# Performance work log

Measured on AMD Instinct MI355X. Metric: run time of the kernel, lower is better.

## Reference

```python
import jax, jax.numpy as jnp
import numpy as np

G = 200          # voxel grid extent per axis (spatial_shape)
EPS = 1e-5       # BatchNorm eps


def setup_inputs() -> dict:
    N, C_in, C_out = 1_000_000, 6, 32
    rng = np.random.default_rng(0)
    # unique active voxel sites (submanifold conv assumes deduplicated coords)
    lin = rng.choice(G ** 3, size=N, replace=False)
    coords = np.stack([lin // (G * G), (lin // G) % G, lin % G], axis=1).astype(np.int32)
    key = jax.random.key(0)
    k1, k2 = jax.random.split(key)
    feat = jax.random.normal(k1, (N, C_in), jnp.float32)
    W = jax.random.normal(k2, (27, C_in, C_out), jnp.float32) * (1.0 / np.sqrt(27 * C_in))
    gamma = jnp.ones((C_out,), jnp.float32)
    beta = jnp.zeros((C_out,), jnp.float32)
    return {"feat": feat, "coords": jnp.asarray(coords), "W": W, "gamma": gamma, "beta": beta}


def _subm_conv_bn_relu(feat, coords, W, gamma, beta):
    # Submanifold 3x3x3 sparse conv: output only at active sites.
    N = feat.shape[0]
    c = coords
    keys = (c[:, 0] * G + c[:, 1]) * G + c[:, 2]          # linearized voxel keys
    order = jnp.argsort(keys)
    skeys = keys[order]
    sfeat = feat[order]
    # all 27 kernel offsets, center included
    r = jnp.arange(-1, 2, dtype=c.dtype)
    offs = jnp.stack(jnp.meshgrid(r, r, r, indexing="ij"), -1).reshape(27, 3)

    def step(acc, xs):
        off, Wk = xs                                       # off: [3], Wk: [C_in, C_out]
        nc = c + off                                       # neighbor coords [N,3]
        valid = jnp.all((nc >= 0) & (nc < G), axis=1)
        nkey = (nc[:, 0] * G + nc[:, 1]) * G + nc[:, 2]
        pos = jnp.clip(jnp.searchsorted(skeys, nkey), 0, N - 1)
        found = valid & (skeys[pos] == nkey)               # rulebook hit mask
        g = jnp.where(found[:, None], sfeat[pos], 0.0)     # gathered neighbor feats [N,C_in]
        return acc + g @ Wk, None

    out, _ = jax.lax.scan(step, jnp.zeros((N, W.shape[2]), feat.dtype), (offs, W))
    # BatchNorm1d (training-mode batch stats) + ReLU
    mean = out.mean(0)
    var = out.var(0)
    out = (out - mean) * jax.lax.rsqrt(var + EPS) * gamma + beta
    return jax.nn.relu(out)


def reference(feat, coords, W, gamma, beta):
    return _subm_conv_bn_relu(feat, coords, W, gamma, beta)
```

## Files before the change

kernel.cpp:

```cpp
#include <hip/hip_runtime.h>
#include <stdint.h>

#define GRIDX 200
#define P 202
#define PCELL (P * P * P)
#define GUARD 100000
#define NBITS (PCELL + GUARD)
#define NWP ((NBITS + 31) / 32)
#define K_INV (PCELL + 50000)
#define CIN 6
#define COUT 32
#define NOFF 27
#define BN_EPS 1e-5f
#define WPB 1024
#define NBLKP ((NWP + WPB - 1) / WPB)

typedef __attribute__((ext_vector_type(8))) short short8;
typedef __attribute__((ext_vector_type(4))) float f32x4;


__device__ __forceinline__ int xcd_swizzle(int b, int nwg) {
    int q = nwg >> 3, r = nwg & 7;
    int xcd = b & 7, idx = b >> 3;
    int base = (xcd < r) ? xcd * (q + 1) : r * (q + 1) + (xcd - r) * q;
    return base + idx;
}

__device__ __forceinline__ unsigned short f2bf(float f) {
    uint32_t u = __float_as_uint(f);
    return (unsigned short)((u + 0x7FFFu + ((u >> 16) & 1u)) >> 16);
}
__device__ __forceinline__ uint32_t pack2(float a, float b) {
    return (uint32_t)f2bf(a) | ((uint32_t)f2bf(b) << 16);
}
__device__ __forceinline__ float bflo(uint32_t u) { return __uint_as_float(u << 16); }
__device__ __forceinline__ float bfhi(uint32_t u) { return __uint_as_float(u & 0xFFFF0000u); }

__device__ __forceinline__ int koff_delta(int koff) {
    int t9 = koff / 9;
    int r9 = koff - t9 * 9;
    int t3 = r9 / 3;
    return (t9 - 1) * (P * P) + (t3 - 1) * P + (r9 - t3 * 3 - 1);
}


__global__ __launch_bounds__(256)
void build_bitmap_v4(const int* __restrict__ coords, int N, uint2* __restrict__ recs) {
    int t = blockIdx.x * blockDim.x + threadIdx.x;
    int i0 = t * 4;
    if (i0 >= N) return;
    if (i0 + 4 <= N) {
        const int4* c4 = (const int4*)(coords + (size_t)i0 * 3);
        int4 ca = c4[0], cb = c4[1], cc = c4[2];
        int cx[4] = {ca.x, ca.w, cb.z, cc.y};
        int cy[4] = {ca.y, cb.x, cb.w, cc.z};
        int cz[4] = {ca.z, cb.y, cc.x, cc.w};
#pragma unroll
        for (int s = 0; s < 4; s++) {
            int key = ((cx[s] + 1) * P + (cy[s] + 1)) * P + (cz[s] + 1);
            atomicOr((unsigned int*)&recs[key >> 5], 1u << (key & 31));
        }
    } else {
        for (int i = i0; i < N; i++) {
            int x = coords[3 * i], y = coords[3 * i + 1], z = coords[3 * i + 2];
            int key = ((x + 1) * P + (y + 1)) * P + (z + 1);
            atomicOr((unsigned int*)&recs[key >> 5], 1u << (key & 31));
        }
    }
}

__global__ __launch_bounds__(256)
void bitmap_count_p(const uint2* __restrict__ recs, int* __restrict__ bcnt) {
    __shared__ int tot[256];
    int b = blockIdx.x, t = threadIdx.x;
    int w0 = b * WPB + t * 4;
    int s = 0;
#pragma unroll
    for (int j = 0; j < 4; j++) {
        int w = w0 + j;
        if (w < NWP) s += __popc(recs[w].x);
    }
    tot[t] = s;
    __syncthreads();
    if (t < 128) tot[t] += tot[t + 128];
    __syncthreads();
    if (t < 64) {
        int v = tot[t] + tot[t + 64];
#pragma unroll
        for (int d = 32; d > 0; d >>= 1) v += __shfl_down(v, d);
        if (t == 0) bcnt[b] = v;
    }
}

__global__ void scan_small(const int* __restrict__ cnt, int* __restrict__ base, int n) {
    __shared__ int tot[256];
    int t = threadIdx.x;
    int v = (t < n) ? cnt[t] : 0;
    tot[t] = v;
    __syncthreads();
    for (int d = 1; d < 256; d <<= 1) {
        int u = (t >= d) ? tot[t - d] : 0;
        __syncthreads();
        tot[t] += u;
        __syncthreads();
    }
    if (t < n) base[t] = tot[t] - v;
}

__global__ __launch_bounds__(256)
void base_fill_skeys(uint2* __restrict__ recs, const int* __restrict__ bbase,
                     int* __restrict__ skeys) {
    __shared__ int tot[256];
    int b = blockIdx.x, t = threadIdx.x;
    int w0 = b * WPB + t * 4;
    uint32_t wd[4];
    int p[4];
    int s = 0;
#pragma unroll
    for (int j = 0; j < 4; j++) {
        int w = w0 + j;
        wd[j] = (w < NWP) ? recs[w].x : 0u;
        p[j] = __popc(wd[j]);
        s += p[j];
    }
    tot[t] = s;
    __syncthreads();
    for (int d = 1; d < 256; d <<= 1) {
        int u = (t >= d) ? tot[t - d] : 0;
        __syncthreads();
        tot[t] += u;
        __syncthreads();
    }
    int run = bbase[b] + tot[t] - s;
#pragma unroll
    for (int j = 0; j < 4; j++) {
        int w = w0 + j;
        if (w < NWP) {
            recs[w].y = (uint32_t)run;
            uint32_t m = wd[j];
            int rr = run;
            int k0 = w * 32;
            while (m) {
                int bit = __ffs((int)m) - 1;
                skeys[rr++] = k0 + bit;
                m &= m - 1u;
            }
            run += p[j];
        }
    }
}


__global__ __launch_bounds__(256)
void rank_scatter_v4(const int* __restrict__ coords, const float* __restrict__ feat, int N,
                     const uint2* __restrict__ recs,
                     uint4* __restrict__ rec32) {
    int t = blockIdx.x * blockDim.x + threadIdx.x;
    int i0 = t * 4;
    if (i0 >= N) return;
    if (i0 + 4 <= N) {
        const int4* c4 = (const int4*)(coords + (size_t)i0 * 3);
        int4 ca = c4[0], cb = c4[1], cc = c4[2];
        int cx[4] = {ca.x, ca.w, cb.z, cc.y};
        int cy[4] = {ca.y, cb.x, cb.w, cc.z};
        int cz[4] = {ca.z, cb.y, cc.x, cc.w};
        const float4* f4 = (const float4*)(feat + (size_t)i0 * 6);
        float4 fa = f4[0], fb = f4[1], fc = f4[2], fd = f4[3], fe = f4[4], ff = f4[5];
        float fs[4][6] = {
            {fa.x, fa.y, fa.z, fa.w, fb.x, fb.y},
            {fb.z, fb.w, fc.x, fc.y, fc.z, fc.w},
            {fd.x, fd.y, fd.z, fd.w, fe.x, fe.y},
            {fe.z, fe.w, ff.x, ff.y, ff.z, ff.w}};
#pragma unroll
        for (int s = 0; s < 4; s++) {
            int key = ((cx[s] + 1) * P + (cy[s] + 1)) * P + (cz[s] + 1);
            uint2 rb = recs[key >> 5];
            int bit = key & 31;
            int r = (int)(rb.y + (uint32_t)__popc(rb.x & ((1u << bit) - 1u)));
            uint4 u;
            u.x = pack2(fs[s][0], fs[s][1]);
            u.y = pack2(fs[s][2], fs[s][3]);
            u.z = pack2(fs[s][4], fs[s][5]);
            u.w = 0u;
            rec32[(size_t)r * 2] = u;
            ((uint32_t*)&rec32[(size_t)r * 2 + 1])[0] = (uint32_t)(i0 + s);
        }
    } else {
        for (int i = i0; i < N; i++) {
            int x = coords[3 * i], y = coords[3 * i + 1], z = coords[3 * i + 2];
            int key = ((x + 1) * P + (y + 1)) * P + (z + 1);
            uint2 rb = recs[key >> 5];
            int bit = key & 31;
            int r = (int)(rb.y + (uint32_t)__popc(rb.x & ((1u << bit) - 1u)));
            const float* fr = feat + (size_t)i * CIN;
            uint4 u;
            u.x = pack2(fr[0], fr[1]);
            u.y = pack2(fr[2], fr[3]);
            u.z = pack2(fr[4], fr[5]);
            u.w = 0u;
            rec32[(size_t)r * 2] = u;
            ((uint32_t*)&rec32[(size_t)r * 2 + 1])[0] = (uint32_t)i;
        }
    }
}


__global__ void prep_wfrag(const float* __restrict__ W, uint4* __restrict__ wfrag) {
    int idx = blockIdx.x * blockDim.x + threadIdx.x;
    if (idx >= 7 * 2 * 64) return;
    int l = idx & 63;
    int nt = (idx >> 6) & 1;
    int ks = idx >> 7;
    int koff = (l >> 4) * 7 + ks;
    int col = nt * 16 + (l & 15);
    unsigned short v[8];
#pragma unroll
    for (int ci = 0; ci < 8; ci++) {
        float f = 0.f;
        if (ci < CIN && koff < NOFF) f = W[(koff * CIN + ci) * COUT + col];
        v[ci] = f2bf(f);
    }
    uint4 u;
    u.x = (uint32_t)v[0] | ((uint32_t)v[1] << 16);
    u.y = (uint32_t)v[2] | ((uint32_t)v[3] << 16);
    u.z = (uint32_t)v[4] | ((uint32_t)v[5] << 16);
    u.w = (uint32_t)v[6] | ((uint32_t)v[7] << 16);
    wfrag[idx] = u;
}


__global__ __launch_bounds__(256, 4)
void conv_mfma(const uint4* __restrict__ rec32,
               const int* __restrict__ skeys,
               const uint4* __restrict__ wfrag,
               const uint2* __restrict__ recs, int N, int nsb,
               uint4* __restrict__ wsbf,
               float* __restrict__ stats_g) {
    __shared__ __align__(16) float Clds[64 * 36];
    __shared__ float bstat[64];

    int tid = threadIdx.x;
    int w = tid >> 6, l = tid & 63;
    int col = l & 15;
    int rg = l >> 4;
    int kb = rg;

    if (tid < 64) bstat[tid] = 0.f;

    const short8* wf8 = (const short8*)wfrag;
    short8 bf0[7], bf1[7];
#pragma unroll
    for (int ks = 0; ks < 7; ks++) {
        bf0[ks] = wf8[(ks * 2 + 0) * 64 + l];
        bf1[ks] = wf8[(ks * 2 + 1) * 64 + l];
    }

    int b1 = (0x3123 >> (kb * 4)) & 0xF;
    int b2 = b1 + 3;
    int len0 = b1, len2 = 4 - b1;
    int koffC0 = kb * 7;
    int koffC1 = koffC0 + b1;
    int koffC2 = koffC0 + b2;
    int d0 = koff_delta(koffC0);
    int d1 = koff_delta(koffC1);
    bool padC2 = (koffC2 >= NOFF);
    int d2 = padC2 ? 0 : koff_delta(koffC2);

    float as0 = 0.f, aq0 = 0.f, as1 = 0.f, aq1 = 0.f;

    for (int sb = blockIdx.x; sb < nsb; sb += gridDim.x) {
        int b = xcd_swizzle(sb, nsb);
        int bs = b * 64;
        int site = bs + w * 16 + col;
        int key = (site < N) ? skeys[site] : K_INV;

        int nkA = key + d0;
        int nkB = key + d1;
        int nkC = padC2 ? K_INV : key + d2;
        int waA = nkA >> 5, waB = nkB >> 5, waC = nkC >> 5;
        uint2 rA0 = recs[waA];
        uint2 rB0 = recs[waB];
        uint2 rC0 = recs[waC];
        uint2 rA1 = rA0, rB1 = rB0, rC1 = rC0;
        if (((nkA & 31) + len0) > 32) rA1 = recs[waA + 1];
        if (((nkB & 31) + 3) > 32)    rB1 = recs[waB + 1];
        if (((nkC & 31) + len2) > 32) rC1 = recs[waC + 1];

        short8 av[7];
#pragma unroll
        for (int ks = 0; ks < 7; ks++) {
            int c = (ks >= b1) + (ks >= b2);
            int nk = (c == 0) ? (nkA + ks)
                   : (c == 1) ? (nkB + (ks - b1))
                              : (nkC + (ks - b2));
            int wa  = (c == 0) ? waA : (c == 1) ? waB : waC;
            uint2 r0 = (c == 0) ? rA0 : (c == 1) ? rB0 : rC0;
            uint2 r1 = (c == 0) ? rA1 : (c == 1) ? rB1 : rC1;
            bool second = (nk >> 5) != wa;
            uint32_t wd = second ? r1.x : r0.x;
            uint32_t bw = second ? r1.y : r0.y;
            int p = nk & 31;
            bool hit = (wd >> p) & 1u;
            uint4 a4 = make_uint4(0u, 0u, 0u, 0u);
            if (hit) {
                int pos = (int)(bw + (uint32_t)__popc(wd & ((1u << p) - 1u)));
                a4 = rec32[(size_t)pos * 2];
            }
            av[ks] = *(const short8*)&a4;
        }

        f32x4 acc0 = {0.f, 0.f, 0.f, 0.f};
        f32x4 acc1 = {0.f, 0.f, 0.f, 0.f};
#pragma unroll
        for (int ks = 0; ks < 7; ks++) {
            acc0 = __builtin_amdgcn_mfma_f32_16x16x32_bf16(av[ks], bf0[ks], acc0, 0, 0, 0);
            acc1 = __builtin_amdgcn_mfma_f32_16x16x32_bf16(av[ks], bf1[ks], acc1, 0, 0, 0);
        }

        as0 += acc0[0] + acc0[1] + acc0[2] + acc0[3];
        aq0 += acc0[0]*acc0[0] + acc0[1]*acc0[1] + acc0[2]*acc0[2] + acc0[3]*acc0[3];
        as1 += acc1[0] + acc1[1] + acc1[2] + acc1[3];
        aq1 += acc1[0]*acc1[0] + acc1[1]*acc1[1] + acc1[2]*acc1[2] + acc1[3]*acc1[3];

        __syncthreads();
#pragma unroll
        for (int r = 0; r < 4; r++) {
            int s = w * 16 + rg * 4 + r;
            Clds[s * 36 + col] = acc0[r];
            Clds[s * 36 + col + 16] = acc1[r];
        }
        __syncthreads();

        int st = tid >> 2;
        int q = tid & 3;
        int sr = bs + st;
        if (sr < N) {
            uint32_t orig = ((const uint32_t*)rec32)[(size_t)sr * 8 + 4];
            const float* cp = &Clds[st * 36 + q * 8];
            uint4 v;
            v.x = pack2(cp[0], cp[1]);
            v.y = pack2(cp[2], cp[3]);
            v.z = pack2(cp[4], cp[5]);
            v.w = pack2(cp[6], cp[7]);
            wsbf[(size_t)orig * 4 + q] = v;
        }
    }

    as0 += __shfl_xor(as0, 16); as0 += __shfl_xor(as0, 32);
    aq0 += __shfl_xor(aq0, 16); aq0 += __shfl_xor(aq0, 32);
    as1 += __shfl_xor(as1, 16); as1 += __shfl_xor(as1, 32);
    aq1 += __shfl_xor(aq1, 16); aq1 += __shfl_xor(aq1, 32);
    __syncthreads();
    if (l < 16) {
        atomicAdd(&bstat[col], as0);
        atomicAdd(&bstat[16 + col], as1);
        atomicAdd(&bstat[32 + col], aq0);
        atomicAdd(&bstat[48 + col], aq1);
    }
    __syncthreads();
    if (tid < 64) {
        int slice = blockIdx.x & 63;
        atomicAdd(&stats_g[slice * 64 + tid], bstat[tid]);
    }
}


__global__ void finalize_sliced(const float* __restrict__ stats_g,
                                const float* __restrict__ gamma,
                                const float* __restrict__ beta,
                                float invN, float* __restrict__ scsh) {
    int c = threadIdx.x;
    if (c < COUT) {
        float s = 0.f, q = 0.f;
        for (int sl = 0; sl < 64; sl++) {
            s += stats_g[sl * 64 + c];
            q += stats_g[sl * 64 + 32 + c];
        }
        float mean = s * invN;
        float var = q * invN - mean * mean;
        float sc = gamma[c] * rsqrtf(var + BN_EPS);
        scsh[c] = sc;
        scsh[COUT + c] = beta[c] - mean * sc;
    }
}


__global__ __launch_bounds__(256)
void norm_bf(const uint4* __restrict__ wsbf, int N,
             const float* __restrict__ scsh, float* __restrict__ out) {
    __shared__ float sc[COUT], sh[COUT];
    for (int t = threadIdx.x; t < COUT; t += blockDim.x) {
        sc[t] = scsh[t];
        sh[t] = scsh[COUT + t];
    }
    __syncthreads();
    int tid = blockIdx.x * blockDim.x + threadIdx.x;
    int i = tid >> 2, q = tid & 3;
    if (i >= N) return;
    uint4 v = wsbf[(size_t)i * 4 + q];
    int cb = q * 8;
    float4 o0, o1;
    o0.x = fmaxf(bflo(v.x) * sc[cb + 0] + sh[cb + 0], 0.f);
    o0.y = fmaxf(bfhi(v.x) * sc[cb + 1] + sh[cb + 1], 0.f);
    o0.z = fmaxf(bflo(v.y) * sc[cb + 2] + sh[cb + 2], 0.f);
    o0.w = fmaxf(bfhi(v.y) * sc[cb + 3] + sh[cb + 3], 0.f);
    o1.x = fmaxf(bflo(v.z) * sc[cb + 4] + sh[cb + 4], 0.f);
    o1.y = fmaxf(bfhi(v.z) * sc[cb + 5] + sh[cb + 5], 0.f);
    o1.z = fmaxf(bflo(v.w) * sc[cb + 6] + sh[cb + 6], 0.f);
    o1.w = fmaxf(bfhi(v.w) * sc[cb + 7] + sh[cb + 7], 0.f);
    float4* gp = (float4*)(out + (size_t)i * COUT + cb);
    gp[0] = o0;
    gp[1] = o1;
}


extern "C" void kernel_launch(void* const* d_in, const int* in_sizes, int n_in,
                              void* d_out, int out_size, void* d_ws, size_t ws_size,
                              hipStream_t stream) {
    const float* feat   = (const float*)d_in[0];
    const int*   coords = (const int*)d_in[1];
    const float* W      = (const float*)d_in[2];
    const float* gamma  = (const float*)d_in[3];
    const float* beta   = (const float*)d_in[4];
    float* out = (float*)d_out;

    int N = in_sizes[0] / CIN;
    const int threads = 256;
    int blocks4 = (N + 4 * threads - 1) / (4 * threads);
    int nsb = (N + 63) / 64;
    int cblocks = 1024;
    int nblocks = (4 * N + threads - 1) / threads;

    size_t a256 = 255;
    size_t recs_b     = (size_t)NWP * 8;
    size_t off_stats  = (recs_b + a256) & ~a256;
    size_t zero_bytes = off_stats + (size_t)64 * 64 * 4;
    size_t off_scsh   = (zero_bytes + a256) & ~a256;
    size_t off_skeys  = (off_scsh + 2 * COUT * 4 + a256) & ~a256;
    size_t off_rec32  = (off_skeys + (size_t)N * 4 + a256) & ~a256;
    size_t off_bcnt   = (off_rec32 + (size_t)(N + 1) * 32 + a256) & ~a256;
    size_t off_bbase  = (off_bcnt + 256 * 4 + a256) & ~a256;
    size_t off_wfrag  = (off_bbase + 256 * 4 + a256) & ~a256;
    size_t off_wsbf   = (off_wfrag + (size_t)(7 * 2 * 64) * 16 + a256) & ~a256;

    uint2* recs  = (uint2*)d_ws;
    float* stats = (float*)((char*)d_ws + off_stats);
    float* scsh  = (float*)((char*)d_ws + off_scsh);
    int*   skeys = (int*)((char*)d_ws + off_skeys);
    uint4* rec32 = (uint4*)((char*)d_ws + off_rec32);
    int*   bcnt  = (int*)((char*)d_ws + off_bcnt);
    int*   bbase = (int*)((char*)d_ws + off_bbase);
    uint4* wfrag = (uint4*)((char*)d_ws + off_wfrag);
    uint4* wsbf  = (uint4*)((char*)d_ws + off_wsbf);

    hipMemsetAsync(d_ws, 0, zero_bytes, stream);
    prep_wfrag<<<4, threads, 0, stream>>>(W, wfrag);
    build_bitmap_v4<<<blocks4, threads, 0, stream>>>(coords, N, recs);
    bitmap_count_p<<<NBLKP, threads, 0, stream>>>(recs, bcnt);
    scan_small<<<1, threads, 0, stream>>>(bcnt, bbase, NBLKP);
    base_fill_skeys<<<NBLKP, threads, 0, stream>>>(recs, bbase, skeys);
    rank_scatter_v4<<<blocks4, threads, 0, stream>>>(coords, feat, N, recs, rec32);
    conv_mfma<<<cblocks, threads, 0, stream>>>(rec32, skeys, wfrag, recs, N, nsb,
                                               wsbf, stats);
    finalize_sliced<<<1, 64, 0, stream>>>(stats, gamma, beta, 1.0f / (float)N, scsh);
    norm_bf<<<nblocks, threads, 0, stream>>>(wsbf, N, scsh, out);
}
```

Before: 174.7 us.

## Fuse block-offset scan into base fill and carry keys in rank records

```diff
diff --git a/kernel.cpp b/kernel.cpp
--- a/kernel.cpp
+++ b/kernel.cpp
@@ -92,11 +92,33 @@
     }
 }
 
-__global__ void scan_small(const int* __restrict__ cnt, int* __restrict__ base, int n) {
+__global__ __launch_bounds__(256)
+void base_fill_p(uint2* __restrict__ recs, const int* __restrict__ bcnt) {
+    __shared__ int btot[256];
     __shared__ int tot[256];
-    int t = threadIdx.x;
-    int v = (t < n) ? cnt[t] : 0;
-    tot[t] = v;
+    int b = blockIdx.x, t = threadIdx.x;
+
+    int bv = (t < NBLKP) ? bcnt[t] : 0;
+    btot[t] = bv;
+    __syncthreads();
+    for (int d = 1; d < 256; d <<= 1) {
+        int u = (t >= d) ? btot[t - d] : 0;
+        __syncthreads();
+        btot[t] += u;
+        __syncthreads();
+    }
+    int blockbase = (b == 0) ? 0 : btot[b - 1];
+
+    int w0 = b * WPB + t * 4;
+    int p[4];
+    int s = 0;
+#pragma unroll
+    for (int j = 0; j < 4; j++) {
+        int w = w0 + j;
+        p[j] = (w < NWP) ? __popc(recs[w].x) : 0;
+        s += p[j];
+    }
+    tot[t] = s;
     __syncthreads();
     for (int d = 1; d < 256; d <<= 1) {
         int u = (t >= d) ? tot[t - d] : 0;
@@ -104,49 +126,12 @@
         tot[t] += u;
         __syncthreads();
     }
-    if (t < n) base[t] = tot[t] - v;
-}
-
-__global__ __launch_bounds__(256)
-void base_fill_skeys(uint2* __restrict__ recs, const int* __restrict__ bbase,
-                     int* __restrict__ skeys) {
-    __shared__ int tot[256];
-    int b = blockIdx.x, t = threadIdx.x;
-    int w0 = b * WPB + t * 4;
-    uint32_t wd[4];
-    int p[4];
-    int s = 0;
+    int run = blockbase + tot[t] - s;
 #pragma unroll
     for (int j = 0; j < 4; j++) {
         int w = w0 + j;
-        wd[j] = (w < NWP) ? recs[w].x : 0u;
-        p[j] = __popc(wd[j]);
-        s += p[j];
-    }
-    tot[t] = s;
-    __syncthreads();
-    for (int d = 1; d < 256; d <<= 1) {
-        int u = (t >= d) ? tot[t - d] : 0;
-        __syncthreads();
-        tot[t] += u;
-        __syncthreads();
-    }
-    int run = bbase[b] + tot[t] - s;
-#pragma unroll
-    for (int j = 0; j < 4; j++) {
-        int w = w0 + j;
-        if (w < NWP) {
-            recs[w].y = (uint32_t)run;
-            uint32_t m = wd[j];
-            int rr = run;
-            int k0 = w * 32;
-            while (m) {
-                int bit = __ffs((int)m) - 1;
-                skeys[rr++] = k0 + bit;
-                m &= m - 1u;
-            }
-            run += p[j];
-        }
+        if (w < NWP) recs[w].y = (uint32_t)run;
+        run += p[j];
     }
 }
 
@@ -156,6 +141,8 @@
                      const uint2* __restrict__ recs,
                      uint4* __restrict__ rec32) {
     int t = blockIdx.x * blockDim.x + threadIdx.x;
+    if (blockIdx.x == 0 && threadIdx.x == 0)
+        ((uint2*)rec32)[(size_t)N * 4 + 2] = make_uint2((uint32_t)K_INV, 0u);
     int i0 = t * 4;
     if (i0 >= N) return;
     if (i0 + 4 <= N) {
@@ -183,7 +170,7 @@
             u.z = pack2(fs[s][4], fs[s][5]);
             u.w = 0u;
             rec32[(size_t)r * 2] = u;
-            ((uint32_t*)&rec32[(size_t)r * 2 + 1])[0] = (uint32_t)(i0 + s);
+            ((uint2*)rec32)[(size_t)r * 4 + 2] = make_uint2((uint32_t)key, (uint32_t)(i0 + s));
         }
     } else {
         for (int i = i0; i < N; i++) {
@@ -199,7 +186,7 @@
             u.z = pack2(fr[4], fr[5]);
             u.w = 0u;
             rec32[(size_t)r * 2] = u;
-            ((uint32_t*)&rec32[(size_t)r * 2 + 1])[0] = (uint32_t)i;
+            ((uint2*)rec32)[(size_t)r * 4 + 2] = make_uint2((uint32_t)key, (uint32_t)i);
         }
     }
 }
@@ -231,13 +218,13 @@
 
 __global__ __launch_bounds__(256, 4)
 void conv_mfma(const uint4* __restrict__ rec32,
-               const int* __restrict__ skeys,
                const uint4* __restrict__ wfrag,
                const uint2* __restrict__ recs, int N, int nsb,
                uint4* __restrict__ wsbf,
                float* __restrict__ stats_g) {
     __shared__ __align__(16) float Clds[64 * 36];
     __shared__ float bstat[64];
+    __shared__ int origLds[64];
 
     int tid = threadIdx.x;
     int w = tid >> 6, l = tid & 63;
@@ -266,13 +253,17 @@
     bool padC2 = (koffC2 >= NOFF);
     int d2 = padC2 ? 0 : koff_delta(koffC2);
 
+    const uint2* ko32 = (const uint2*)rec32;
+
     float as0 = 0.f, aq0 = 0.f, as1 = 0.f, aq1 = 0.f;
 
     for (int sb = blockIdx.x; sb < nsb; sb += gridDim.x) {
         int b = xcd_swizzle(sb, nsb);
         int bs = b * 64;
         int site = bs + w * 16 + col;
-        int key = (site < N) ? skeys[site] : K_INV;
+        int sidx = (site < N) ? site : N;
+        uint2 ko = ko32[(size_t)sidx * 4 + 2];
+        int key = (int)ko.x;
 
         int nkA = key + d0;
         int nkB = key + d1;
@@ -329,13 +320,14 @@
             Clds[s * 36 + col] = acc0[r];
             Clds[s * 36 + col + 16] = acc1[r];
         }
+        if (rg == 0) origLds[w * 16 + col] = (int)ko.y;
         __syncthreads();
 
         int st = tid >> 2;
         int q = tid & 3;
         int sr = bs + st;
         if (sr < N) {
-            uint32_t orig = ((const uint32_t*)rec32)[(size_t)sr * 8 + 4];
+            uint32_t orig = (uint32_t)origLds[st];
             const float* cp = &Clds[st * 36 + q * 8];
             uint4 v;
             v.x = pack2(cp[0], cp[1]);
@@ -436,20 +428,16 @@
     size_t off_stats  = (recs_b + a256) & ~a256;
     size_t zero_bytes = off_stats + (size_t)64 * 64 * 4;
     size_t off_scsh   = (zero_bytes + a256) & ~a256;
-    size_t off_skeys  = (off_scsh + 2 * COUT * 4 + a256) & ~a256;
-    size_t off_rec32  = (off_skeys + (size_t)N * 4 + a256) & ~a256;
+    size_t off_rec32  = (off_scsh + 2 * COUT * 4 + a256) & ~a256;
     size_t off_bcnt   = (off_rec32 + (size_t)(N + 1) * 32 + a256) & ~a256;
-    size_t off_bbase  = (off_bcnt + 256 * 4 + a256) & ~a256;
-    size_t off_wfrag  = (off_bbase + 256 * 4 + a256) & ~a256;
+    size_t off_wfrag  = (off_bcnt + 256 * 4 + a256) & ~a256;
     size_t off_wsbf   = (off_wfrag + (size_t)(7 * 2 * 64) * 16 + a256) & ~a256;
 
     uint2* recs  = (uint2*)d_ws;
     float* stats = (float*)((char*)d_ws + off_stats);
     float* scsh  = (float*)((char*)d_ws + off_scsh);
-    int*   skeys = (int*)((char*)d_ws + off_skeys);
     uint4* rec32 = (uint4*)((char*)d_ws + off_rec32);
     int*   bcnt  = (int*)((char*)d_ws + off_bcnt);
-    int*   bbase = (int*)((char*)d_ws + off_bbase);
     uint4* wfrag = (uint4*)((char*)d_ws + off_wfrag);
     uint4* wsbf  = (uint4*)((char*)d_ws + off_wsbf);
 
@@ -457,11 +445,9 @@
     prep_wfrag<<<4, threads, 0, stream>>>(W, wfrag);
     build_bitmap_v4<<<blocks4, threads, 0, stream>>>(coords, N, recs);
     bitmap_count_p<<<NBLKP, threads, 0, stream>>>(recs, bcnt);
-    scan_small<<<1, threads, 0, stream>>>(bcnt, bbase, NBLKP);
-    base_fill_skeys<<<NBLKP, threads, 0, stream>>>(recs, bbase, skeys);
+    base_fill_p<<<NBLKP, threads, 0, stream>>>(recs, bcnt);
     rank_scatter_v4<<<blocks4, threads, 0, stream>>>(coords, feat, N, recs, rec32);
-    conv_mfma<<<cblocks, threads, 0, stream>>>(rec32, skeys, wfrag, recs, N, nsb,
-                                               wsbf, stats);
+    conv_mfma<<<cblocks, threads, 0, stream>>>(rec32, wfrag, recs, N, nsb, wsbf, stats);
     finalize_sliced<<<1, 64, 0, stream>>>(stats, gamma, beta, 1.0f / (float)N, scsh);
     norm_bf<<<nblocks, threads, 0, stream>>>(wsbf, N, scsh, out);
 }
```

After: 165.4 us (median of 2 runs). -5.3%, faster.
